# Performance work log

Measured on AMD Instinct MI355X. Metric: run time of the kernel, lower is better.

Reference implementation:

```python
import jax, jax.numpy as jnp
import numpy as np

B, T, C = 2, 2048, 2048
H, HKV = 32, 8
D = C // H            # head_dim = 64
G = H // HKV          # groups = 4
ROPE_BASE = 10000.0


def _rotate_half(x):
    x1, x2 = jnp.split(x, 2, axis=-1)
    return jnp.concatenate((-x2, x1), axis=-1)


def _rope_tables(seq_len, dim):
    inv_freq = 1.0 / (ROPE_BASE ** (jnp.arange(0, dim, 2, dtype=jnp.float32) / dim))
    t = jnp.arange(seq_len, dtype=jnp.float32)
    freqs = jnp.outer(t, inv_freq)          # [T, D/2]
    emb = jnp.concatenate((freqs, freqs), axis=-1)  # [T, D]
    return jnp.cos(emb), jnp.sin(emb)


def setup_inputs() -> dict:
    key = jax.random.key(0)
    ks = jax.random.split(key, 5)
    s = 0.02
    return {
        "x": jax.random.normal(ks[0], (B, T, C), jnp.float32),
        "Wq": jax.random.normal(ks[1], (C, C), jnp.float32) * s,
        "Wk": jax.random.normal(ks[2], (HKV * D, C), jnp.float32) * s,
        "Wv": jax.random.normal(ks[3], (HKV * D, C), jnp.float32) * s,
        "Wo": jax.random.normal(ks[4], (C, C), jnp.float32) * s,
    }


def reference(x, Wq, Wk, Wv, Wo):
    b, t, c = x.shape
    # fused QKV projections (nn.Linear: y = x @ W.T)
    q = (x @ Wq.T).reshape(b, t, H, D).transpose(0, 2, 1, 3)      # [B,H,T,D]
    k = (x @ Wk.T).reshape(b, t, HKV, D).transpose(0, 2, 1, 3)    # [B,HKV,T,D]
    v = (x @ Wv.T).reshape(b, t, HKV, D).transpose(0, 2, 1, 3)

    # RoPE (start_pos = 0)
    cos, sin = _rope_tables(t, D)           # [T, D] each
    cos = cos[None, None]                   # [1,1,T,D]
    sin = sin[None, None]
    q = q * cos + _rotate_half(q) * sin
    k = k * cos + _rotate_half(k) * sin

    # GQA head expansion (repeat_interleave on head dim)
    k = jnp.repeat(k, G, axis=1)            # [B,H,T,D]
    v = jnp.repeat(v, G, axis=1)

    # causal attention
    scale = 1.0 / jnp.sqrt(jnp.asarray(D, jnp.float32))
    scores = jnp.einsum('bhqd,bhkd->bhqk', q, k) * scale          # [B,H,T,T]
    causal = jnp.tril(jnp.ones((t, t), dtype=bool))
    scores = jnp.where(causal[None, None], scores, -jnp.inf)
    attn = jax.nn.softmax(scores.astype(jnp.float32), axis=-1).astype(q.dtype)
    out = jnp.einsum('bhqk,bhkd->bhqd', attn, v)                  # [B,H,T,D]
    out = out.transpose(0, 2, 1, 3).reshape(b, t, c)
    return out @ Wo.T
```

## Files before the change

kernel.cpp:

```cpp
#include <hip/hip_runtime.h>
#include <hip/hip_bf16.h>
#include <math.h>

typedef short short8 __attribute__((ext_vector_type(8)));
typedef float floatx4 __attribute__((ext_vector_type(4)));
typedef unsigned int uintx4 __attribute__((ext_vector_type(4)));
typedef int intx2 __attribute__((ext_vector_type(2)));

typedef __attribute__((address_space(1))) unsigned int as1_u32;
typedef __attribute__((address_space(3))) unsigned int as3_u32;

__device__ __forceinline__ void load_lds16(const void* g, void* l) {
  __builtin_amdgcn_global_load_lds((const as1_u32*)g, (as3_u32*)l, 16, 0, 0);
}

__device__ __forceinline__ unsigned short f2bf(float f) {
  __bf16 h = (__bf16)f;
  return __builtin_bit_cast(unsigned short, h);
}

__device__ __forceinline__ unsigned int pack_bf16(float a, float b) {
  return (unsigned int)f2bf(a) | ((unsigned int)f2bf(b) << 16);
}

#define MFMA16(a, b, c) __builtin_amdgcn_mfma_f32_16x16x32_bf16(a, b, c, 0, 0, 0)

#define TB 2
#define TT 2048
#define TC 2048
#define QKN 2560
#define KOFF 2048
#define SCALE_Q 0.18033688f

__global__ __launch_bounds__(256) void cast_all(
    const float* __restrict__ x, const float* __restrict__ wq,
    const float* __restrict__ wk, const float* __restrict__ wv,
    const float* __restrict__ wo,
    unsigned short* __restrict__ xb, unsigned short* __restrict__ wqkv,
    unsigned short* __restrict__ wob, float2* __restrict__ ropeTab) {
  if (blockIdx.x < 256) {
    const int idx = blockIdx.x * 256 + threadIdx.x;
    const int t = idx >> 5, d = idx & 31;
    const float inv = exp2f((float)d * -0.4152410119f);
    float sn, cs;
    sincosf((float)t * inv, &sn, &cs);
    ropeTab[idx] = make_float2(cs, sn);
  }
  long i4 = (long)blockIdx.x * 256 + threadIdx.x;
  const float* src;
  unsigned short* dst;
  if (i4 < 2097152)      { src = x;  dst = xb; }
  else if (i4 < 3145728) { src = wq; dst = wqkv;           i4 -= 2097152; }
  else if (i4 < 3407872) { src = wk; dst = wqkv + 4194304; i4 -= 3145728; }
  else if (i4 < 3670016) { src = wv; dst = wqkv + 5242880; i4 -= 3407872; }
  else                   { src = wo; dst = wob;            i4 -= 3670016; }
  float4 v = ((const float4*)src)[i4];
  ushort4 o;
  o.x = f2bf(v.x); o.y = f2bf(v.y); o.z = f2bf(v.z); o.w = f2bf(v.w);
  ((ushort4*)dst)[i4] = o;
}

#define MFMA_QUAD(I0, J0, BF)                                                  \
  __builtin_amdgcn_s_setprio(1);                                               \
  _Pragma("unroll") for (int i_ = 0; i_ < 4; ++i_) {                           \
    _Pragma("unroll") for (int j_ = 0; j_ < 2; ++j_) {                         \
      acc[(I0) + i_][(J0) + j_] =                                              \
          MFMA16(af[i_][0], BF[j_][0], acc[(I0) + i_][(J0) + j_]);             \
      acc[(I0) + i_][(J0) + j_] =                                              \
          MFMA16(af[i_][1], BF[j_][1], acc[(I0) + i_][(J0) + j_]);             \
    }                                                                          \
  }                                                                            \
  __builtin_amdgcn_s_setprio(0);

__device__ __forceinline__ void gemm256_8ph(
    const unsigned short* __restrict__ A, const unsigned short* __restrict__ Bw,
    char* dynlds, int m0, int n0, int K, floatx4 (&acc)[8][4]) {
  const int tid = threadIdx.x;
  const int lane = tid & 63;
  const int w = tid >> 6;
  const int quad = lane >> 4, l15 = lane & 15;
  const int wm = w >> 2, wn = w & 3;

  const int srow8 = tid >> 3;
  const int schk = (tid & 7) ^ (srow8 & 7);
  const unsigned short* aS = A + (size_t)(m0 + srow8) * K + schk * 8;
  const unsigned short* bS = Bw + (size_t)(n0 + srow8) * K + schk * 8;

  const int key0 = (quad ^ (l15 & 7)) << 4;
  const int key1 = ((4 + quad) ^ (l15 & 7)) << 4;
  const int rdA = (wm * 16 + l15) * 128;
  const int rdB = 32768 + ((wn >> 1) * 64 + (wn & 1) * 16 + l15) * 128;

  const int NIT = K >> 7;

  auto stage = [&](int bb, int isB, int h, int tt) {
    char* d = dynlds + bb * 65536 + isB * 32768 + h * 16384;
    const unsigned short* s = (isB ? bS : aS) + (size_t)tt * 64 + (size_t)(h * 128) * K;
    load_lds16(s, d + tid * 16);
    load_lds16(s + (size_t)64 * K, d + 8192 + tid * 16);
  };

  stage(0, 0, 0, 0); stage(0, 1, 0, 0); stage(0, 1, 1, 0); stage(0, 0, 1, 0);
  stage(1, 0, 0, 1); stage(1, 1, 1, 1);
  asm volatile("s_waitcnt vmcnt(4)" ::: "memory");
  __builtin_amdgcn_s_barrier();

  short8 af[4][2], bfA[2][2], bfB[2][2];
  const char* cb0 = dynlds;
  const char* cb1 = dynlds + 65536;

  for (int it = 0; it < NIT; ++it) {
    const int tO = it * 2 + 1, tE2 = it * 2 + 2, tO2 = it * 2 + 3;
    const bool STG = (it < NIT - 1);

#pragma unroll
    for (int i = 0; i < 4; ++i) {
      af[i][0] = *(const short8*)(cb0 + rdA + i * 4096 + key0);
      af[i][1] = *(const short8*)(cb0 + rdA + i * 4096 + key1);
    }
#pragma unroll
    for (int j = 0; j < 2; ++j) {
      bfA[j][0] = *(const short8*)(cb0 + rdB + j * 4096 + key0);
      bfA[j][1] = *(const short8*)(cb0 + rdB + j * 4096 + key1);
    }
    stage(1, 1, 0, tO);
    __builtin_amdgcn_s_barrier();
    asm volatile("s_waitcnt lgkmcnt(0)" ::: "memory");
    MFMA_QUAD(0, 0, bfA)
    __builtin_amdgcn_s_barrier();

#pragma unroll
    for (int j = 0; j < 2; ++j) {
      bfB[j][0] = *(const short8*)(cb0 + rdB + 16384 + j * 4096 + key0);
      bfB[j][1] = *(const short8*)(cb0 + rdB + 16384 + j * 4096 + key1);
    }
    stage(1, 0, 1, tO);
    __builtin_amdgcn_s_barrier();
    asm volatile("s_waitcnt lgkmcnt(0)" ::: "memory");
    MFMA_QUAD(0, 2, bfB)
    __builtin_amdgcn_s_barrier();

#pragma unroll
    for (int i = 0; i < 4; ++i) {
      af[i][0] = *(const short8*)(cb0 + rdA + (i + 4) * 4096 + key0);
      af[i][1] = *(const short8*)(cb0 + rdA + (i + 4) * 4096 + key1);
    }
    if (STG) stage(0, 0, 0, tE2);
    __builtin_amdgcn_s_barrier();
    asm volatile("s_waitcnt lgkmcnt(0)" ::: "memory");
    MFMA_QUAD(4, 2, bfB)
    __builtin_amdgcn_s_barrier();

    if (STG) stage(0, 1, 1, tE2);
    MFMA_QUAD(4, 0, bfA)
    if (STG) asm volatile("s_waitcnt vmcnt(4)" ::: "memory");
    else     asm volatile("s_waitcnt vmcnt(0)" ::: "memory");
    __builtin_amdgcn_s_barrier();

#pragma unroll
    for (int i = 0; i < 4; ++i) {
      af[i][0] = *(const short8*)(cb1 + rdA + i * 4096 + key0);
      af[i][1] = *(const short8*)(cb1 + rdA + i * 4096 + key1);
    }
#pragma unroll
    for (int j = 0; j < 2; ++j) {
      bfA[j][0] = *(const short8*)(cb1 + rdB + j * 4096 + key0);
      bfA[j][1] = *(const short8*)(cb1 + rdB + j * 4096 + key1);
    }
    if (STG) stage(0, 1, 0, tE2);
    __builtin_amdgcn_s_barrier();
    asm volatile("s_waitcnt lgkmcnt(0)" ::: "memory");
    MFMA_QUAD(0, 0, bfA)
    __builtin_amdgcn_s_barrier();

#pragma unroll
    for (int j = 0; j < 2; ++j) {
      bfB[j][0] = *(const short8*)(cb1 + rdB + 16384 + j * 4096 + key0);
      bfB[j][1] = *(const short8*)(cb1 + rdB + 16384 + j * 4096 + key1);
    }
    if (STG) stage(0, 0, 1, tE2);
    __builtin_amdgcn_s_barrier();
    asm volatile("s_waitcnt lgkmcnt(0)" ::: "memory");
    MFMA_QUAD(0, 2, bfB)
    __builtin_amdgcn_s_barrier();

#pragma unroll
    for (int i = 0; i < 4; ++i) {
      af[i][0] = *(const short8*)(cb1 + rdA + (i + 4) * 4096 + key0);
      af[i][1] = *(const short8*)(cb1 + rdA + (i + 4) * 4096 + key1);
    }
    if (STG) stage(1, 0, 0, tO2);
    __builtin_amdgcn_s_barrier();
    asm volatile("s_waitcnt lgkmcnt(0)" ::: "memory");
    MFMA_QUAD(4, 2, bfB)
    __builtin_amdgcn_s_barrier();

    if (STG) stage(1, 1, 1, tO2);
    MFMA_QUAD(4, 0, bfA)
    if (STG) asm volatile("s_waitcnt vmcnt(4)" ::: "memory");
    else     asm volatile("s_waitcnt vmcnt(0)" ::: "memory");
    __builtin_amdgcn_s_barrier();
  }
}

#define OUTCOL(n0, wn, j, l15) \
  ((n0) + ((j) >> 1) * 128 + ((wn) >> 1) * 64 + ((wn) & 1) * 16 + ((j) & 1) * 32 + (l15))

__global__ __launch_bounds__(512, 2) void gemm_qkv(const unsigned short* __restrict__ A,
                                                   const unsigned short* __restrict__ Bw,
                                                   unsigned short* __restrict__ qk,
                                                   unsigned short* __restrict__ vT,
                                                   const float2* __restrict__ ropeTab) {
  extern __shared__ char dynlds[];
  const int K = 2048;
  const int tid = threadIdx.x;
  const int lane = tid & 63, w = tid >> 6;
  const int quad = lane >> 4, l15 = lane & 15;
  const int wm = w >> 2, wn = w & 3;

  const int lin = blockIdx.y * 12 + blockIdx.x;
  const int wg = (lin & 7) * 24 + (lin >> 3);
  const int m0 = (wg / 12) * 256;
  const int n0 = (wg % 12) * 256;

  floatx4 acc[8][4];
#pragma unroll
  for (int i = 0; i < 8; ++i)
#pragma unroll
    for (int j = 0; j < 4; ++j) acc[i][j] = (floatx4){0.f, 0.f, 0.f, 0.f};

  gemm256_8ph(A, Bw, dynlds, m0, n0, K, acc);

  if (n0 < QKN) {
    const float qscale = (n0 < KOFF) ? SCALE_Q : 1.0f;
    const int d = (wn & 1) * 16 + l15;
#pragma unroll
    for (int i = 0; i < 8; ++i) {
      const int rowb = m0 + i * 32 + wm * 16 + quad * 4;
      const int tb = rowb & (TT - 1);
#pragma unroll
      for (int jp = 0; jp < 4; jp += 2) {
        const int col = OUTCOL(n0, wn, jp, l15);
#pragma unroll
        for (int r = 0; r < 4; ++r) {
          const float2 cssn = ropeTab[(tb + r) * 32 + d];
          const float a = acc[i][jp][r], b2 = acc[i][jp + 1][r];
          const float qa = (a * cssn.x - b2 * cssn.y) * qscale;
          const float qb = (b2 * cssn.x + a * cssn.y) * qscale;
          unsigned short* p = qk + (size_t)(rowb + r) * QKN + col;
          p[0] = f2bf(qa);
          p[32] = f2bf(qb);
        }
      }
    }
  } else {
#pragma unroll
    for (int i = 0; i < 8; ++i) {
      const int rowb = m0 + i * 32 + wm * 16 + quad * 4;
#pragma unroll
      for (int j = 0; j < 4; ++j) {
        const int col = OUTCOL(n0, wn, j, l15);
        ushort4 pk;
        pk.x = f2bf(acc[i][j][0]); pk.y = f2bf(acc[i][j][1]);
        pk.z = f2bf(acc[i][j][2]); pk.w = f2bf(acc[i][j][3]);
        *(ushort4*)(vT + (size_t)(col - 2560) * 4096 + rowb) = pk;
      }
    }
  }
}

#define NT_MFMA(J0, BF)                                                        \
  __builtin_amdgcn_s_setprio(1);                                               \
  _Pragma("unroll") for (int i_ = 0; i_ < 4; ++i_) {                           \
    _Pragma("unroll") for (int j_ = 0; j_ < 2; ++j_) {                         \
      acc[i_][(J0) + j_] = MFMA16(af[i_][0], BF[j_][0], acc[i_][(J0) + j_]);   \
      acc[i_][(J0) + j_] = MFMA16(af[i_][1], BF[j_][1], acc[i_][(J0) + j_]);   \
    }                                                                          \
  }                                                                            \
  __builtin_amdgcn_s_setprio(0);

__global__ __launch_bounds__(512, 2) void gemm_nt_f32(const unsigned short* __restrict__ A,
                                                      const unsigned short* __restrict__ Bw,
                                                      float* __restrict__ C,
                                                      int M, int N, int Kdim) {
  extern __shared__ char dynlds[];
  const int K = 2048;
  const int tid = threadIdx.x;
  const int lane = tid & 63, w = tid >> 6;
  const int quad = lane >> 4, l15 = lane & 15;
  const int wm = w >> 1, wn = w & 1;

  const int lin = blockIdx.y * 16 + blockIdx.x;
  const int wg = (lin & 7) * 32 + (lin >> 3);
  const int m0 = (wg >> 4) * 256;
  const int n0 = (wg & 15) * 128;

  floatx4 acc[4][4];
#pragma unroll
  for (int i = 0; i < 4; ++i)
#pragma unroll
    for (int j = 0; j < 4; ++j) acc[i][j] = (floatx4){0.f, 0.f, 0.f, 0.f};

  const int srow8 = tid >> 3;
  const int schk = (tid & 7) ^ (srow8 & 7);
  const unsigned short* aS = A + (size_t)(m0 + srow8) * K + schk * 8;
  const unsigned short* bS = Bw + (size_t)(n0 + srow8) * K + schk * 8;

  const int key0 = (quad ^ (l15 & 7)) << 4;
  const int key1 = ((4 + quad) ^ (l15 & 7)) << 4;
  const int rdA = (wm * 64 + l15) * 128;
  const int rdB = 32768 + (wn * 64 + l15) * 128;

  auto stage = [&](int bb, int slot, int tt) {
    char* d = dynlds + bb * 49152 + slot * 16384;
    const unsigned short* s =
        (slot == 2 ? bS : aS + (size_t)(slot * 128) * K) + (size_t)tt * 64;
    load_lds16(s, d + tid * 16);
    load_lds16(s + (size_t)64 * K, d + 8192 + tid * 16);
  };

  stage(0, 0, 0); stage(0, 1, 0); stage(0, 2, 0);
  stage(1, 0, 1); stage(1, 1, 1);
  asm volatile("s_waitcnt vmcnt(4)" ::: "memory");
  __builtin_amdgcn_s_barrier();

  short8 af[4][2], bfL[2][2], bfR[2][2];
  const char* cb0 = dynlds;
  const char* cb1 = dynlds + 49152;
  const int NIT = K >> 7;

  for (int it = 0; it < NIT; ++it) {
    const int tO = it * 2 + 1, tE2 = it * 2 + 2, tO2 = it * 2 + 3;
    const bool STG = (it < NIT - 1);

#pragma unroll
    for (int i = 0; i < 4; ++i) {
      af[i][0] = *(const short8*)(cb0 + rdA + i * 2048 + key0);
      af[i][1] = *(const short8*)(cb0 + rdA + i * 2048 + key1);
    }
#pragma unroll
    for (int j = 0; j < 2; ++j) {
      bfL[j][0] = *(const short8*)(cb0 + rdB + j * 2048 + key0);
      bfL[j][1] = *(const short8*)(cb0 + rdB + j * 2048 + key1);
    }
    stage(1, 2, tO);
    __builtin_amdgcn_s_barrier();
    asm volatile("s_waitcnt lgkmcnt(0)" ::: "memory");
    NT_MFMA(0, bfL)
    __builtin_amdgcn_s_barrier();

#pragma unroll
    for (int j = 0; j < 2; ++j) {
      bfR[j][0] = *(const short8*)(cb0 + rdB + (2 + j) * 2048 + key0);
      bfR[j][1] = *(const short8*)(cb0 + rdB + (2 + j) * 2048 + key1);
    }
    if (STG) {
      stage(0, 0, tE2); stage(0, 1, tE2);
      asm volatile("s_waitcnt vmcnt(4)" ::: "memory");
    } else {
      asm volatile("s_waitcnt vmcnt(0)" ::: "memory");
    }
    __builtin_amdgcn_s_barrier();
    asm volatile("s_waitcnt lgkmcnt(0)" ::: "memory");
    NT_MFMA(2, bfR)
    __builtin_amdgcn_s_barrier();

#pragma unroll
    for (int i = 0; i < 4; ++i) {
      af[i][0] = *(const short8*)(cb1 + rdA + i * 2048 + key0);
      af[i][1] = *(const short8*)(cb1 + rdA + i * 2048 + key1);
    }
#pragma unroll
    for (int j = 0; j < 2; ++j) {
      bfL[j][0] = *(const short8*)(cb1 + rdB + j * 2048 + key0);
      bfL[j][1] = *(const short8*)(cb1 + rdB + j * 2048 + key1);
    }
    if (STG) stage(0, 2, tE2);
    __builtin_amdgcn_s_barrier();
    asm volatile("s_waitcnt lgkmcnt(0)" ::: "memory");
    NT_MFMA(0, bfL)
    __builtin_amdgcn_s_barrier();

#pragma unroll
    for (int j = 0; j < 2; ++j) {
      bfR[j][0] = *(const short8*)(cb1 + rdB + (2 + j) * 2048 + key0);
      bfR[j][1] = *(const short8*)(cb1 + rdB + (2 + j) * 2048 + key1);
    }
    if (STG) {
      stage(1, 0, tO2); stage(1, 1, tO2);
      asm volatile("s_waitcnt vmcnt(4)" ::: "memory");
    } else {
      asm volatile("s_waitcnt vmcnt(0)" ::: "memory");
    }
    __builtin_amdgcn_s_barrier();
    asm volatile("s_waitcnt lgkmcnt(0)" ::: "memory");
    NT_MFMA(2, bfR)
    __builtin_amdgcn_s_barrier();
  }

#pragma unroll
  for (int i = 0; i < 4; ++i) {
    const int row = m0 + wm * 64 + i * 16 + quad * 4;
#pragma unroll
    for (int j = 0; j < 4; ++j) {
      const int col = n0 + wn * 64 + j * 16 + l15;
#pragma unroll
      for (int r = 0; r < 4; ++r)
        C[(size_t)(row + r) * N + col] = acc[i][j][r];
    }
  }
}

__global__ __launch_bounds__(256, 3) void attn_kernel(const unsigned short* __restrict__ qk,
                                                      const unsigned short* __restrict__ vT,
                                                      unsigned short* __restrict__ attn) {
  const int h = blockIdx.x, b = blockIdx.y;
  const int qt = 15 - (int)blockIdx.z;
  const int hk = h >> 2;
  const int tid = threadIdx.x;
  const int w = tid >> 6, lane = tid & 63, quad = lane >> 4, l15 = lane & 15;

  __shared__ char lds[32768];

  const int srow = tid >> 3;
  const int sgrp = ((tid & 7) ^ (srow & 7));
  const int relbase = w * 32 + l15;

  const short8 ones = {16256, 16256, 16256, 16256, 16256, 16256, 16256, 16256};

  const size_t rowQ = (size_t)(b * TT + qt * 128);

  {
    const unsigned short* qsrc = qk + (rowQ + srow) * QKN + h * 64 + sgrp * 8;
#pragma unroll
    for (int p = 0; p < 4; ++p)
      load_lds16(qsrc + (size_t)p * 32 * QKN, lds + p * 4096 + tid * 16);
  }
  __syncthreads();
  short8 qf[2][2];
#pragma unroll
  for (int i = 0; i < 2; ++i)
#pragma unroll
    for (int ks = 0; ks < 2; ++ks)
      qf[i][ks] = *(const short8*)(lds + (w * 32 + i * 16 + l15) * 128 +
                                   ((((ks << 2) + quad) ^ (l15 & 7)) << 4));
  __syncthreads();

  floatx4 accO[2][4], accL[2];
#pragma unroll
  for (int i = 0; i < 2; ++i) {
    accL[i] = (floatx4){0.f, 0.f, 0.f, 0.f};
#pragma unroll
    for (int j = 0; j < 4; ++j) accO[i][j] = (floatx4){0.f, 0.f, 0.f, 0.f};
  }

  const unsigned short* kptr =
      qk + (size_t)(b * TT + srow) * QKN + KOFF + hk * 64 + sgrp * 8;
  const unsigned short* vptr =
      vT + (size_t)(hk * 64 + srow) * 4096 + b * TT + sgrp * 8;

  load_lds16(kptr, lds + tid * 16);
  load_lds16(kptr + (size_t)32 * QKN, lds + 4096 + tid * 16);
  load_lds16(vptr, lds + 16384 + tid * 16);
  load_lds16(vptr + (size_t)32 * 4096, lds + 16384 + 4096 + tid * 16);
  kptr += (size_t)64 * QKN;
  vptr += 64;
  __syncthreads();

  auto step = [&](const int BUF, const bool PREF, const int MREL) {
    if (PREF) {
      char* kd = lds + ((BUF ^ 1) * 8192);
      char* vd = lds + 16384 + ((BUF ^ 1) * 8192);
      load_lds16(kptr, kd + tid * 16);
      load_lds16(kptr + (size_t)32 * QKN, kd + 4096 + tid * 16);
      load_lds16(vptr, vd + tid * 16);
      load_lds16(vptr + (size_t)32 * 4096, vd + 4096 + tid * 16);
      kptr += (size_t)64 * QKN;
      vptr += 64;
    }

    const char* Ks = lds + BUF * 8192;
    floatx4 st[2][4];
    __builtin_amdgcn_s_setprio(1);
#pragma unroll
    for (int jm = 0; jm < 4; ++jm) {
      const int krow = jm * 16 + l15;
      const short8 kf0 = *(const short8*)(Ks + krow * 128 + ((quad ^ (l15 & 7)) << 4));
      const short8 kf1 = *(const short8*)(Ks + krow * 128 + (((4 + quad) ^ (l15 & 7)) << 4));
#pragma unroll
      for (int i = 0; i < 2; ++i) {
        floatx4 z = (floatx4){0.f, 0.f, 0.f, 0.f};
        z = __builtin_amdgcn_mfma_f32_16x16x32_bf16(kf0, qf[i][0], z, 0, 0, 0);
        st[i][jm] = __builtin_amdgcn_mfma_f32_16x16x32_bf16(kf1, qf[i][1], z, 0, 0, 0);
      }
    }
    __builtin_amdgcn_s_setprio(0);

    const char* Vt = lds + 16384 + BUF * 8192;
    short8 vf[2][4];
#pragma unroll
    for (int ks = 0; ks < 2; ++ks)
#pragma unroll
      for (int jd = 0; jd < 4; ++jd) {
        const int d = jd * 16 + l15;
        vf[ks][jd] = *(const short8*)(Vt + d * 128 +
                                      ((((ks << 2) + quad) ^ (l15 & 7)) << 4));
      }

    short8 pT[2][2];
#pragma unroll
    for (int i = 0; i < 2; ++i) {
      unsigned int U[4][2];
#pragma unroll
      for (int jm = 0; jm < 4; ++jm) {
        float e0 = __builtin_amdgcn_exp2f(st[i][jm][0]);
        float e1 = __builtin_amdgcn_exp2f(st[i][jm][1]);
        float e2 = __builtin_amdgcn_exp2f(st[i][jm][2]);
        float e3 = __builtin_amdgcn_exp2f(st[i][jm][3]);
        if (MREL >= 0) {
          const int rel = relbase + i * 16 - MREL;
          const int kg = jm * 16 + quad * 4;
          if (kg > rel) e0 = 0.f;
          if (kg + 1 > rel) e1 = 0.f;
          if (kg + 2 > rel) e2 = 0.f;
          if (kg + 3 > rel) e3 = 0.f;
        }
        U[jm][0] = pack_bf16(e0, e1);
        U[jm][1] = pack_bf16(e2, e3);
      }
#pragma unroll
      for (int ks = 0; ks < 2; ++ks) {
        uintx4 t;
#pragma unroll
        for (int hh = 0; hh < 2; ++hh) {
          intx2 r32 = __builtin_amdgcn_permlane32_swap(
              (int)U[2 * ks][hh], (int)U[2 * ks + 1][hh], false, false);
          intx2 r16 = __builtin_amdgcn_permlane16_swap(r32[0], r32[1], false, false);
          t[hh] = (unsigned int)r16[0];
          t[2 + hh] = (unsigned int)r16[1];
        }
        pT[i][ks] = __builtin_bit_cast(short8, t);
      }
    }

    __builtin_amdgcn_s_setprio(1);
#pragma unroll
    for (int ks = 0; ks < 2; ++ks) {
      accL[0] = __builtin_amdgcn_mfma_f32_16x16x32_bf16(pT[0][ks], ones, accL[0], 0, 0, 0);
      accL[1] = __builtin_amdgcn_mfma_f32_16x16x32_bf16(pT[1][ks], ones, accL[1], 0, 0, 0);
#pragma unroll
      for (int jd = 0; jd < 4; ++jd) {
        accO[0][jd] = __builtin_amdgcn_mfma_f32_16x16x32_bf16(pT[0][ks], vf[ks][jd], accO[0][jd], 0, 0, 0);
        accO[1][jd] = __builtin_amdgcn_mfma_f32_16x16x32_bf16(pT[1][ks], vf[ks][jd], accO[1][jd], 0, 0, 0);
      }
    }
    __builtin_amdgcn_s_setprio(0);
    __syncthreads();
  };

  for (int t2 = 0; t2 < qt; ++t2) {
    step(0, true, -1);
    step(1, true, -1);
  }
  step(0, true, 0);
  step(1, false, 64);

#pragma unroll
  for (int i2 = 0; i2 < 2; ++i2) {
    floatx4 rl;
#pragma unroll
    for (int r = 0; r < 4; ++r) rl[r] = __builtin_amdgcn_rcpf(accL[i2][r]);
#pragma unroll
    for (int jd = 0; jd < 4; ++jd) {
      const int col = h * 64 + jd * 16 + l15;
#pragma unroll
      for (int r = 0; r < 4; ++r) {
        const size_t row = rowQ + w * 32 + i2 * 16 + quad * 4 + r;
        attn[row * TC + col] = f2bf(accO[i2][jd][r] * rl[r]);
      }
    }
  }
}

extern "C" void kernel_launch(void* const* d_in, const int* in_sizes, int n_in,
                              void* d_out, int out_size, void* d_ws, size_t ws_size,
                              hipStream_t stream) {
  const float* x = (const float*)d_in[0];
  const float* Wq = (const float*)d_in[1];
  const float* Wk = (const float*)d_in[2];
  const float* Wv = (const float*)d_in[3];
  const float* Wo = (const float*)d_in[4];
  float* out = (float*)d_out;

  char* ws = (char*)d_ws;
  unsigned short* xb   = (unsigned short*)(ws);
  unsigned short* wqkv = (unsigned short*)(ws + 16777216);
  unsigned short* wob  = (unsigned short*)(ws + 29360128);
  unsigned short* qk   = (unsigned short*)(ws + 37748736);
  unsigned short* vT   = (unsigned short*)(ws + 58720256);
  unsigned short* attn = (unsigned short*)(ws + 62914560);
  float2* ropeTab = (float2*)(ws + 62914560);

  cast_all<<<18432, 256, 0, stream>>>(x, Wq, Wk, Wv, Wo, xb, wqkv, wob, ropeTab);
  gemm_qkv<<<dim3(12, 16), 512, 131072, stream>>>(xb, wqkv, qk, vT, ropeTab);
  attn_kernel<<<dim3(32, 2, 16), 256, 0, stream>>>(qk, vT, attn);
  gemm_nt_f32<<<dim3(16, 16), 512, 98304, stream>>>(attn, wob, out, 4096, TC, 2048);
}
```

Before: 249.3 us.

## Retile QKV GEMM to 256x192 tiles with a new warp layout

The QKV projection GEMM moves from 256x256 tiles (192 workgroups) to 256x192 tiles (256 workgroups), giving better coverage of the GPU's compute units. Warps are rearranged into a 4x2 grid, each computing 64x96, and the B fragments are permuted so that RoPE pairs (d and d+32) stay in the same thread. The pipeline is rebuilt with separate A and B staging and four phases per iteration. The epilogue now picks RoPE or the V-transpose store per column block, which adds branching, and the LDS footprint shrinks.

```diff
diff --git a/kernel.cpp b/kernel.cpp
--- a/kernel.cpp
+++ b/kernel.cpp
@@ -60,151 +60,15 @@
   ((ushort4*)dst)[i4] = o;
 }
 
-#define MFMA_QUAD(I0, J0, BF)                                                  \
+#define QKV_MFMA(BF)                                                           \
   __builtin_amdgcn_s_setprio(1);                                               \
   _Pragma("unroll") for (int i_ = 0; i_ < 4; ++i_) {                           \
-    _Pragma("unroll") for (int j_ = 0; j_ < 2; ++j_) {                         \
-      acc[(I0) + i_][(J0) + j_] =                                              \
-          MFMA16(af[i_][0], BF[j_][0], acc[(I0) + i_][(J0) + j_]);             \
-      acc[(I0) + i_][(J0) + j_] =                                              \
-          MFMA16(af[i_][1], BF[j_][1], acc[(I0) + i_][(J0) + j_]);             \
+    _Pragma("unroll") for (int j_ = 0; j_ < 3; ++j_) {                         \
+      acc[i_][JBASE + j_] = MFMA16(af[i_][0], BF[j_][0], acc[i_][JBASE + j_]); \
+      acc[i_][JBASE + j_] = MFMA16(af[i_][1], BF[j_][1], acc[i_][JBASE + j_]); \
     }                                                                          \
   }                                                                            \
   __builtin_amdgcn_s_setprio(0);
-
-__device__ __forceinline__ void gemm256_8ph(
-    const unsigned short* __restrict__ A, const unsigned short* __restrict__ Bw,
-    char* dynlds, int m0, int n0, int K, floatx4 (&acc)[8][4]) {
-  const int tid = threadIdx.x;
-  const int lane = tid & 63;
-  const int w = tid >> 6;
-  const int quad = lane >> 4, l15 = lane & 15;
-  const int wm = w >> 2, wn = w & 3;
-
-  const int srow8 = tid >> 3;
-  const int schk = (tid & 7) ^ (srow8 & 7);
-  const unsigned short* aS = A + (size_t)(m0 + srow8) * K + schk * 8;
-  const unsigned short* bS = Bw + (size_t)(n0 + srow8) * K + schk * 8;
-
-  const int key0 = (quad ^ (l15 & 7)) << 4;
-  const int key1 = ((4 + quad) ^ (l15 & 7)) << 4;
-  const int rdA = (wm * 16 + l15) * 128;
-  const int rdB = 32768 + ((wn >> 1) * 64 + (wn & 1) * 16 + l15) * 128;
-
-  const int NIT = K >> 7;
-
-  auto stage = [&](int bb, int isB, int h, int tt) {
-    char* d = dynlds + bb * 65536 + isB * 32768 + h * 16384;
-    const unsigned short* s = (isB ? bS : aS) + (size_t)tt * 64 + (size_t)(h * 128) * K;
-    load_lds16(s, d + tid * 16);
-    load_lds16(s + (size_t)64 * K, d + 8192 + tid * 16);
-  };
-
-  stage(0, 0, 0, 0); stage(0, 1, 0, 0); stage(0, 1, 1, 0); stage(0, 0, 1, 0);
-  stage(1, 0, 0, 1); stage(1, 1, 1, 1);
-  asm volatile("s_waitcnt vmcnt(4)" ::: "memory");
-  __builtin_amdgcn_s_barrier();
-
-  short8 af[4][2], bfA[2][2], bfB[2][2];
-  const char* cb0 = dynlds;
-  const char* cb1 = dynlds + 65536;
-
-  for (int it = 0; it < NIT; ++it) {
-    const int tO = it * 2 + 1, tE2 = it * 2 + 2, tO2 = it * 2 + 3;
-    const bool STG = (it < NIT - 1);
-
-#pragma unroll
-    for (int i = 0; i < 4; ++i) {
-      af[i][0] = *(const short8*)(cb0 + rdA + i * 4096 + key0);
-      af[i][1] = *(const short8*)(cb0 + rdA + i * 4096 + key1);
-    }
-#pragma unroll
-    for (int j = 0; j < 2; ++j) {
-      bfA[j][0] = *(const short8*)(cb0 + rdB + j * 4096 + key0);
-      bfA[j][1] = *(const short8*)(cb0 + rdB + j * 4096 + key1);
-    }
-    stage(1, 1, 0, tO);
-    __builtin_amdgcn_s_barrier();
-    asm volatile("s_waitcnt lgkmcnt(0)" ::: "memory");
-    MFMA_QUAD(0, 0, bfA)
-    __builtin_amdgcn_s_barrier();
-
-#pragma unroll
-    for (int j = 0; j < 2; ++j) {
-      bfB[j][0] = *(const short8*)(cb0 + rdB + 16384 + j * 4096 + key0);
-      bfB[j][1] = *(const short8*)(cb0 + rdB + 16384 + j * 4096 + key1);
-    }
-    stage(1, 0, 1, tO);
-    __builtin_amdgcn_s_barrier();
-    asm volatile("s_waitcnt lgkmcnt(0)" ::: "memory");
-    MFMA_QUAD(0, 2, bfB)
-    __builtin_amdgcn_s_barrier();
-
-#pragma unroll
-    for (int i = 0; i < 4; ++i) {
-      af[i][0] = *(const short8*)(cb0 + rdA + (i + 4) * 4096 + key0);
-      af[i][1] = *(const short8*)(cb0 + rdA + (i + 4) * 4096 + key1);
-    }
-    if (STG) stage(0, 0, 0, tE2);
-    __builtin_amdgcn_s_barrier();
-    asm volatile("s_waitcnt lgkmcnt(0)" ::: "memory");
-    MFMA_QUAD(4, 2, bfB)
-    __builtin_amdgcn_s_barrier();
-
-    if (STG) stage(0, 1, 1, tE2);
-    MFMA_QUAD(4, 0, bfA)
-    if (STG) asm volatile("s_waitcnt vmcnt(4)" ::: "memory");
-    else     asm volatile("s_waitcnt vmcnt(0)" ::: "memory");
-    __builtin_amdgcn_s_barrier();
-
-#pragma unroll
-    for (int i = 0; i < 4; ++i) {
-      af[i][0] = *(const short8*)(cb1 + rdA + i * 4096 + key0);
-      af[i][1] = *(const short8*)(cb1 + rdA + i * 4096 + key1);
-    }
-#pragma unroll
-    for (int j = 0; j < 2; ++j) {
-      bfA[j][0] = *(const short8*)(cb1 + rdB + j * 4096 + key0);
-      bfA[j][1] = *(const short8*)(cb1 + rdB + j * 4096 + key1);
-    }
-    if (STG) stage(0, 1, 0, tE2);
-    __builtin_amdgcn_s_barrier();
-    asm volatile("s_waitcnt lgkmcnt(0)" ::: "memory");
-    MFMA_QUAD(0, 0, bfA)
-    __builtin_amdgcn_s_barrier();
-
-#pragma unroll
-    for (int j = 0; j < 2; ++j) {
-      bfB[j][0] = *(const short8*)(cb1 + rdB + 16384 + j * 4096 + key0);
-      bfB[j][1] = *(const short8*)(cb1 + rdB + 16384 + j * 4096 + key1);
-    }
-    if (STG) stage(0, 0, 1, tE2);
-    __builtin_amdgcn_s_barrier();
-    asm volatile("s_waitcnt lgkmcnt(0)" ::: "memory");
-    MFMA_QUAD(0, 2, bfB)
-    __builtin_amdgcn_s_barrier();
-
-#pragma unroll
-    for (int i = 0; i < 4; ++i) {
-      af[i][0] = *(const short8*)(cb1 + rdA + (i + 4) * 4096 + key0);
-      af[i][1] = *(const short8*)(cb1 + rdA + (i + 4) * 4096 + key1);
-    }
-    if (STG) stage(1, 0, 0, tO2);
-    __builtin_amdgcn_s_barrier();
-    asm volatile("s_waitcnt lgkmcnt(0)" ::: "memory");
-    MFMA_QUAD(4, 2, bfB)
-    __builtin_amdgcn_s_barrier();
-
-    if (STG) stage(1, 1, 1, tO2);
-    MFMA_QUAD(4, 0, bfA)
-    if (STG) asm volatile("s_waitcnt vmcnt(4)" ::: "memory");
-    else     asm volatile("s_waitcnt vmcnt(0)" ::: "memory");
-    __builtin_amdgcn_s_barrier();
-  }
-}
-
-#define OUTCOL(n0, wn, j, l15) \
-  ((n0) + ((j) >> 1) * 128 + ((wn) >> 1) * 64 + ((wn) & 1) * 16 + ((j) & 1) * 32 + (l15))
 
 __global__ __launch_bounds__(512, 2) void gemm_qkv(const unsigned short* __restrict__ A,
                                                    const unsigned short* __restrict__ Bw,
@@ -216,31 +80,153 @@
   const int tid = threadIdx.x;
   const int lane = tid & 63, w = tid >> 6;
   const int quad = lane >> 4, l15 = lane & 15;
-  const int wm = w >> 2, wn = w & 3;
-
-  const int lin = blockIdx.y * 12 + blockIdx.x;
-  const int wg = (lin & 7) * 24 + (lin >> 3);
-  const int m0 = (wg / 12) * 256;
-  const int n0 = (wg % 12) * 256;
-
-  floatx4 acc[8][4];
-#pragma unroll
-  for (int i = 0; i < 8; ++i)
-#pragma unroll
-    for (int j = 0; j < 4; ++j) acc[i][j] = (floatx4){0.f, 0.f, 0.f, 0.f};
-
-  gemm256_8ph(A, Bw, dynlds, m0, n0, K, acc);
-
-  if (n0 < QKN) {
-    const float qscale = (n0 < KOFF) ? SCALE_Q : 1.0f;
-    const int d = (wn & 1) * 16 + l15;
-#pragma unroll
-    for (int i = 0; i < 8; ++i) {
-      const int rowb = m0 + i * 32 + wm * 16 + quad * 4;
-      const int tb = rowb & (TT - 1);
-#pragma unroll
-      for (int jp = 0; jp < 4; jp += 2) {
-        const int col = OUTCOL(n0, wn, jp, l15);
+  const int wm = w >> 1, wn = w & 1;
+
+  const int lin = blockIdx.y * 16 + blockIdx.x;
+  const int wg = (lin & 7) * 32 + (lin >> 3);
+  const int m0 = (wg >> 4) * 256;
+  const int n0 = (wg & 15) * 192;
+
+  floatx4 acc[4][6];
+#pragma unroll
+  for (int i = 0; i < 4; ++i)
+#pragma unroll
+    for (int j = 0; j < 6; ++j) acc[i][j] = (floatx4){0.f, 0.f, 0.f, 0.f};
+
+  const int srow8 = tid >> 3;
+  const int schk = (tid & 7) ^ (srow8 & 7);
+  const unsigned short* aS = A + (size_t)(m0 + srow8) * K + schk * 8;
+  const unsigned short* bS = Bw + (size_t)(n0 + srow8) * K + schk * 8;
+
+  const int key0 = (quad ^ (l15 & 7)) << 4;
+  const int key1 = ((4 + quad) ^ (l15 & 7)) << 4;
+  const int rdA = (wm * 64 + l15) * 128;
+  const int rdBl = 32768 + l15 * 128;
+
+  constexpr int F0[6] = {0, 2, 1, 3, 4, 6};
+  constexpr int F1[6] = {5, 7, 8, 10, 9, 11};
+
+  auto stageA = [&](int bb, int tt) {
+    char* d = dynlds + bb * 57344;
+    const unsigned short* s = aS + (size_t)tt * 64;
+    load_lds16(s, d + tid * 16);
+    load_lds16(s + (size_t)64 * K, d + 8192 + tid * 16);
+    load_lds16(s + (size_t)128 * K, d + 16384 + tid * 16);
+    load_lds16(s + (size_t)192 * K, d + 24576 + tid * 16);
+  };
+  auto stageB = [&](int bb, int tt) {
+    char* d = dynlds + bb * 57344 + 32768;
+    const unsigned short* s = bS + (size_t)tt * 64;
+    load_lds16(s, d + tid * 16);
+    load_lds16(s + (size_t)64 * K, d + 8192 + tid * 16);
+    load_lds16(s + (size_t)128 * K, d + 16384 + tid * 16);
+  };
+
+  stageA(0, 0); stageB(0, 0); stageA(1, 1);
+  asm volatile("s_waitcnt vmcnt(4)" ::: "memory");
+  __builtin_amdgcn_s_barrier();
+
+  short8 af[4][2], bfL[3][2], bfR[3][2];
+  const char* cb0 = dynlds;
+  const char* cb1 = dynlds + 57344;
+  const int NIT = K >> 7;
+
+  for (int it = 0; it < NIT; ++it) {
+    const int tO = it * 2 + 1, tE2 = it * 2 + 2, tO2 = it * 2 + 3;
+    const bool STG = (it < NIT - 1);
+
+#pragma unroll
+    for (int i = 0; i < 4; ++i) {
+      af[i][0] = *(const short8*)(cb0 + rdA + i * 2048 + key0);
+      af[i][1] = *(const short8*)(cb0 + rdA + i * 2048 + key1);
+    }
+#pragma unroll
+    for (int j = 0; j < 3; ++j) {
+      const int fe = wn ? F1[j] : F0[j];
+      bfL[j][0] = *(const short8*)(cb0 + rdBl + fe * 2048 + key0);
+      bfL[j][1] = *(const short8*)(cb0 + rdBl + fe * 2048 + key1);
+    }
+    stageB(1, tO);
+    __builtin_amdgcn_s_barrier();
+    asm volatile("s_waitcnt lgkmcnt(0)" ::: "memory");
+    {
+      const int JBASE = 0;
+      QKV_MFMA(bfL)
+    }
+    __builtin_amdgcn_s_barrier();
+
+#pragma unroll
+    for (int j = 0; j < 3; ++j) {
+      const int fe = wn ? F1[3 + j] : F0[3 + j];
+      bfR[j][0] = *(const short8*)(cb0 + rdBl + fe * 2048 + key0);
+      bfR[j][1] = *(const short8*)(cb0 + rdBl + fe * 2048 + key1);
+    }
+    if (STG) {
+      stageA(0, tE2);
+      asm volatile("s_waitcnt vmcnt(4)" ::: "memory");
+    } else {
+      asm volatile("s_waitcnt vmcnt(0)" ::: "memory");
+    }
+    __builtin_amdgcn_s_barrier();
+    asm volatile("s_waitcnt lgkmcnt(0)" ::: "memory");
+    {
+      const int JBASE = 3;
+      QKV_MFMA(bfR)
+    }
+    __builtin_amdgcn_s_barrier();
+
+#pragma unroll
+    for (int i = 0; i < 4; ++i) {
+      af[i][0] = *(const short8*)(cb1 + rdA + i * 2048 + key0);
+      af[i][1] = *(const short8*)(cb1 + rdA + i * 2048 + key1);
+    }
+#pragma unroll
+    for (int j = 0; j < 3; ++j) {
+      const int fe = wn ? F1[j] : F0[j];
+      bfL[j][0] = *(const short8*)(cb1 + rdBl + fe * 2048 + key0);
+      bfL[j][1] = *(const short8*)(cb1 + rdBl + fe * 2048 + key1);
+    }
+    if (STG) stageB(0, tE2);
+    __builtin_amdgcn_s_barrier();
+    asm volatile("s_waitcnt lgkmcnt(0)" ::: "memory");
+    {
+      const int JBASE = 0;
+      QKV_MFMA(bfL)
+    }
+    __builtin_amdgcn_s_barrier();
+
+#pragma unroll
+    for (int j = 0; j < 3; ++j) {
+      const int fe = wn ? F1[3 + j] : F0[3 + j];
+      bfR[j][0] = *(const short8*)(cb1 + rdBl + fe * 2048 + key0);
+      bfR[j][1] = *(const short8*)(cb1 + rdBl + fe * 2048 + key1);
+    }
+    if (STG) {
+      stageA(1, tO2);
+      asm volatile("s_waitcnt vmcnt(4)" ::: "memory");
+    } else {
+      asm volatile("s_waitcnt vmcnt(0)" ::: "memory");
+    }
+    __builtin_amdgcn_s_barrier();
+    asm volatile("s_waitcnt lgkmcnt(0)" ::: "memory");
+    {
+      const int JBASE = 3;
+      QKV_MFMA(bfR)
+    }
+    __builtin_amdgcn_s_barrier();
+  }
+
+#pragma unroll
+  for (int i = 0; i < 4; ++i) {
+    const int rowb = m0 + wm * 64 + i * 16 + quad * 4;
+    const int tb = rowb & (TT - 1);
+#pragma unroll
+    for (int jp = 0; jp < 6; jp += 2) {
+      const int fe = wn ? F1[jp] : F0[jp];
+      const int col = n0 + fe * 16 + l15;
+      if (col < QKN) {
+        const float qscale = (col < KOFF) ? SCALE_Q : 1.0f;
+        const int d = (fe & 3) * 16 + l15;
 #pragma unroll
         for (int r = 0; r < 4; ++r) {
           const float2 cssn = ropeTab[(tb + r) * 32 + d];
@@ -251,19 +237,16 @@
           p[0] = f2bf(qa);
           p[32] = f2bf(qb);
         }
-      }
-    }
-  } else {
-#pragma unroll
-    for (int i = 0; i < 8; ++i) {
-      const int rowb = m0 + i * 32 + wm * 16 + quad * 4;
-#pragma unroll
-      for (int j = 0; j < 4; ++j) {
-        const int col = OUTCOL(n0, wn, j, l15);
-        ushort4 pk;
-        pk.x = f2bf(acc[i][j][0]); pk.y = f2bf(acc[i][j][1]);
-        pk.z = f2bf(acc[i][j][2]); pk.w = f2bf(acc[i][j][3]);
-        *(ushort4*)(vT + (size_t)(col - 2560) * 4096 + rowb) = pk;
+      } else {
+#pragma unroll
+        for (int jj = jp; jj < jp + 2; ++jj) {
+          const int fv = wn ? F1[jj] : F0[jj];
+          const int colv = n0 + fv * 16 + l15;
+          ushort4 pk;
+          pk.x = f2bf(acc[i][jj][0]); pk.y = f2bf(acc[i][jj][1]);
+          pk.z = f2bf(acc[i][jj][2]); pk.w = f2bf(acc[i][jj][3]);
+          *(ushort4*)(vT + (size_t)(colv - 2560) * 4096 + rowb) = pk;
+        }
       }
     }
   }
@@ -602,7 +585,7 @@
   float2* ropeTab = (float2*)(ws + 62914560);
 
   cast_all<<<18432, 256, 0, stream>>>(x, Wq, Wk, Wv, Wo, xb, wqkv, wob, ropeTab);
-  gemm_qkv<<<dim3(12, 16), 512, 131072, stream>>>(xb, wqkv, qk, vT, ropeTab);
+  gemm_qkv<<<dim3(16, 16), 512, 114688, stream>>>(xb, wqkv, qk, vT, ropeTab);
   attn_kernel<<<dim3(32, 2, 16), 256, 0, stream>>>(qk, vT, attn);
   gemm_nt_f32<<<dim3(16, 16), 512, 98304, stream>>>(attn, wob, out, 4096, TC, 2048);
 }
```

New measurement: 246.4 us. About the same (-1.2%).
